# Kernel optimization log

Measured on AMD Instinct MI355X. Metric: run time of the kernel, lower is better.

## Reference

```python
import jax, jax.numpy as jnp
import numpy as np

# Dimensions matching init_kwargs
B, S, D, d_feat, O = 64, 1024, 64, 2, 10
L = S // 2  # label_site
STD = 0.01  # 'random_eye' init noise scale


def setup_inputs() -> dict:
    key = jax.random.key(0)
    k1, k2, k3, k4 = jax.random.split(key, 4)
    x = jax.random.normal(k1, (B, S, d_feat), dtype=jnp.float32)
    # InputRegion tensors, bond_str 'slri': eye over (l, r) broadcast over (s, i)
    W_left = jnp.eye(D, dtype=jnp.float32)[None, :, :, None] \
        + STD * jax.random.normal(k2, (L, D, D, d_feat), dtype=jnp.float32)
    W_right = jnp.eye(D, dtype=jnp.float32)[None, :, :, None] \
        + STD * jax.random.normal(k3, (S - L, D, D, d_feat), dtype=jnp.float32)
    # OutputSite tensor, bond_str 'olr': eye over (l, r) broadcast over o
    out_core = jnp.eye(D, dtype=jnp.float32)[None, :, :] \
        + STD * jax.random.normal(k4, (O, D, D), dtype=jnp.float32)
    return {"x": x, "W_left": W_left, "out_core": out_core, "W_right": W_right}


def reference(x, W_left, out_core, W_right):
    # x: [B, S, d]; W_left: [L, D, D, d]; out_core: [O, D, D]; W_right: [S-L, D, D, d]
    Ls = W_left.shape[0]
    Dv = W_left.shape[1]
    Bv = x.shape[0]
    # Per-site matrices (einsum 'slri,bsi->bslr'), laid out scan-major [S, B, D, D]
    mats_l = jnp.einsum('slri,bsi->sblr', W_left, x[:, :Ls])
    mats_r = jnp.einsum('slri,bsi->sblr', W_right, x[:, Ls:])
    # Open boundary edge vectors e = [1, 0, ..., 0]
    e = jnp.zeros((Dv,), dtype=x.dtype).at[0].set(1.0)
    v0 = jnp.broadcast_to(e, (Bv, Dv))
    # Left-to-right vector propagation through left chain
    def lstep(v, m):
        return jnp.einsum('bl,blr->br', v, m), None
    vL, _ = jax.lax.scan(lstep, v0, mats_l)
    # Right-to-left vector propagation through right chain
    def rstep(w, m):
        return jnp.einsum('blr,br->bl', m, w), None
    wR, _ = jax.lax.scan(rstep, v0, mats_r, reverse=True)
    # Contract through the output core: [B, O]
    return jnp.einsum('bl,olr,br->bo', vL, out_core, wR)
```

## Files before the change

### kernel.cpp

```cpp
#include <hip/hip_runtime.h>
#include <stdint.h>

#define NSITE 512
#define DD    64
#define NB    64
#define NO    10
#define NSEG  16
#define SEGLEN 32
#define SLAB_BYTES 32768
#define PACK_BYTES 16384

typedef short bf16x8 __attribute__((ext_vector_type(8)));
typedef float f32x16 __attribute__((ext_vector_type(16)));

__device__ __forceinline__ uint32_t pk2(float a, float b) {
    return __builtin_amdgcn_perm(__float_as_uint(b), __float_as_uint(a), 0x07060302);
}

__device__ __forceinline__ float2 pkmul2(float2 a, float2 b) {
    float2 r;
    asm("v_pk_mul_f32 %0, %1, %2" : "=v"(r) : "v"(a), "v"(b));
    return r;
}

__global__ __launch_bounds__(256) void pack_kernel(float* __restrict__ wl,
                                                   float* __restrict__ wr) {
    const int g = blockIdx.x;
    const int right = (g >= NSITE) ? 1 : 0;
    const int s = right ? g - NSITE : g;
    float* base = (right ? wr : wl) + (size_t)s * (SLAB_BYTES / 4);

    __shared__ float2 st[DD * 65];
    const float4* src4 = (const float4*)base;
    for (int e4 = threadIdx.x; e4 < DD * DD / 2; e4 += 256) {
        const float4 v = src4[e4];
        const int e = e4 * 2;
        float2* d = &st[(e >> 6) * 65 + (e & 63)];
        d[0] = make_float2(v.x, v.y);
        d[1] = make_float2(v.z, v.w);
    }
    __syncthreads();

    uint32_t* out = (uint32_t*)base;
    #pragma unroll
    for (int rr = 0; rr < 16; ++rr) {
        const int od = rr * 256 + threadIdx.x;
        const int chunk = od >> 8, i = chunk >> 3, sk = chunk & 7;
        const int H = (od >> 7) & 1, m5 = (od >> 2) & 31, d = od & 3;
        const int m = 32 * i + m5, k = 8 * sk + 4 * H + d;
        const float2 a = right ? st[m * 65 + k] : st[k * 65 + m];
        out[od] = pk2(a.x, a.y);
    }
}

__device__ __forceinline__ void dma16(const void* gp, void* lp) {
    __builtin_amdgcn_global_load_lds(
        (const __attribute__((address_space(1))) uint32_t*)gp,
        (__attribute__((address_space(3))) uint32_t*)lp, 16, 0, 0);
}

__global__ __launch_bounds__(256, 2) void stage1_kernel(
        const float* __restrict__ x, float* __restrict__ wl, float* __restrict__ wr) {
    const int pb   = blockIdx.x;
    const int bid  = (pb & 7) * 64 + (pb >> 3);
    const int side = bid >> 8;
    const int seg  = (bid >> 4) & 15;
    const int bq   = bid & 15;
    const int wave = threadIdx.x >> 6;
    const int lane = threadIdx.x & 63;
    const int b    = bq * 4 + wave;
    const int m5   = lane & 31;
    const int H    = lane >> 5;

    __shared__ __align__(16) char ring[4][PACK_BYTES];
    __shared__ float2 xs[4][SEGLEN];

    char* wbuf = (char*)(side ? wr : wl);

    if (lane < SEGLEN) {
        const float2* xp = ((const float2*)x) + (size_t)b * 1024 + (side ? NSITE : 0);
        const int sg = seg * SEGLEN + (side ? SEGLEN - 1 - lane : lane);
        xs[wave][lane] = xp[sg];
    }

    auto siteAddr = [&](int t) -> const char* {
        const int sg = seg * SEGLEN + (side ? SEGLEN - 1 - t : t);
        return wbuf + (size_t)sg * SLAB_BYTES;
    };

    #pragma unroll
    for (int t0 = 0; t0 < 2; ++t0) {
        const char* sb = siteAddr(t0);
        #pragma unroll
        for (int c = 0; c < 4; ++c) {
            const int ch = wave * 4 + c;
            dma16(sb + ch * 1024 + lane * 16, ring[t0] + ch * 1024);
        }
    }

    f32x16 acc[2][2];
    #pragma unroll
    for (int i = 0; i < 2; ++i)
        #pragma unroll
        for (int j = 0; j < 2; ++j)
            #pragma unroll
            for (int q = 0; q < 16; ++q) {
                const int row = (q & 3) + 8 * (q >> 2) + 4 * H;
                acc[i][j][q] = (i == j && row == m5) ? 1.f : 0.f;
            }

    f32x16 zf;
    #pragma unroll
    for (int q = 0; q < 16; ++q) zf[q] = 0.f;

    union BU { bf16x8 v; uint32_t w[4]; };

    for (int t = 0; t < SEGLEN; ++t) {
        int t2 = t + 2; if (t2 > SEGLEN - 1) t2 = SEGLEN - 1;
        {
            const char* sb = siteAddr(t2);
            char* lb = ring[(t + 2) & 3];
            #pragma unroll
            for (int c = 0; c < 4; ++c) {
                const int ch = wave * 4 + c;
                dma16(sb + ch * 1024 + lane * 16, lb + ch * 1024);
            }
        }
        asm volatile("s_waitcnt vmcnt(8)" ::: "memory");
        asm volatile("s_barrier" ::: "memory");

        const char* rb = ring[t & 3];
        const float2 xv = xs[wave][t];
        const float2 xx = make_float2(xv.x, xv.x);
        const float2 xy = make_float2(xv.y, xv.y);

        BU bfa[8][2];
        #pragma unroll
        for (int sk = 0; sk < 8; ++sk) {
            const int mi = sk >> 2, qb = 4 * (sk & 3);
            #pragma unroll
            for (int j = 0; j < 2; ++j)
                #pragma unroll
                for (int dp = 0; dp < 2; ++dp) {
                    const float2 v01 = make_float2(acc[mi][j][qb + 2 * dp],
                                                   acc[mi][j][qb + 2 * dp + 1]);
                    const float2 pa = pkmul2(xx, v01);
                    const float2 pb = pkmul2(xy, v01);
                    bfa[sk][j].w[2 * dp + 0] = pk2(pa.x, pb.x);
                    bfa[sk][j].w[2 * dp + 1] = pk2(pa.y, pb.y);
                }
        }

        __builtin_amdgcn_s_setprio(1);
        #pragma unroll
        for (int sk = 0; sk < 8; ++sk) {
            #pragma unroll
            for (int i = 0; i < 2; ++i) {
                union { bf16x8 v; uint4 u; } a;
                a.u = *(const uint4*)(rb + (i * 8 + sk) * 1024 + lane * 16);
                #pragma unroll
                for (int j = 0; j < 2; ++j)
                    acc[i][j] = __builtin_amdgcn_mfma_f32_32x32x16_bf16(
                        a.v, bfa[sk][j].v, (sk == 0) ? zf : acc[i][j], 0, 0, 0);
            }
        }
        __builtin_amdgcn_s_setprio(0);
    }

    {
        const int p = b * NSEG + seg;
        char* pdst = wbuf + (size_t)(p >> 1) * SLAB_BYTES + PACK_BYTES + (p & 1) * 8192;
        #pragma unroll
        for (int i = 0; i < 2; ++i)
            #pragma unroll
            for (int j = 0; j < 2; ++j) {
                const int c = 32 * j + m5;
                #pragma unroll
                for (int Q = 0; Q < 4; ++Q) {
                    const int r0 = 32 * i + 8 * Q + 4 * H;
                    uint2 val;
                    val.x = pk2(acc[i][j][4 * Q + 0], acc[i][j][4 * Q + 1]);
                    val.y = pk2(acc[i][j][4 * Q + 2], acc[i][j][4 * Q + 3]);
                    *(uint2*)(pdst + c * 128 + r0 * 2) = val;
                }
            }
    }
    asm volatile("s_waitcnt vmcnt(0)" ::: "memory");
}

__global__ __launch_bounds__(512) void tail_kernel(
        const float* __restrict__ wl, const float* __restrict__ wr,
        const float* __restrict__ core, float* __restrict__ out) {
    const int b    = blockIdx.x;
    const int tid  = threadIdx.x;
    const int side = tid >> 8;
    const int r    = tid & 63;
    const int cg   = (tid >> 6) & 3;
    const char* wbuf = (const char*)(side ? wr : wl);

    __shared__ float vsh[2][DD];
    __shared__ float part[2][4][DD];
    if ((tid & 255) < DD) vsh[side][r] = (r == 0) ? 1.f : 0.f;

    auto Pseg = [&](int gi) -> const uint16_t* {
        const int g = side ? (NSEG - 1 - gi) : gi;
        const int p = b * NSEG + g;
        return (const uint16_t*)(wbuf
            + (size_t)(p >> 1) * SLAB_BYTES + PACK_BYTES + (p & 1) * 8192);
    };

    float pv[16];
    {
        const uint16_t* P = Pseg(0);
        #pragma unroll
        for (int cc = 0; cc < 16; ++cc)
            pv[cc] = __uint_as_float(((uint32_t)P[(cg * 16 + cc) * 64 + r]) << 16);
    }
    __syncthreads();

    for (int gi = 0; gi < NSEG; ++gi) {
        float nv[16];
        const bool more = (gi + 1 < NSEG);
        if (more) {
            const uint16_t* Pn = Pseg(gi + 1);
            #pragma unroll
            for (int cc = 0; cc < 16; ++cc)
                nv[cc] = __uint_as_float(((uint32_t)Pn[(cg * 16 + cc) * 64 + r]) << 16);
        }
        float acc = 0.f;
        #pragma unroll
        for (int cc = 0; cc < 16; ++cc)
            acc = fmaf(vsh[side][cg * 16 + cc], pv[cc], acc);
        part[side][cg][r] = acc;
        asm volatile("s_waitcnt lgkmcnt(0)" ::: "memory");
        __builtin_amdgcn_s_barrier();
        if ((tid & 255) < DD)
            vsh[side][r] = part[side][0][r] + part[side][1][r]
                         + part[side][2][r] + part[side][3][r];
        asm volatile("s_waitcnt lgkmcnt(0)" ::: "memory");
        __builtin_amdgcn_s_barrier();
        if (more) {
            #pragma unroll
            for (int cc = 0; cc < 16; ++cc) pv[cc] = nv[cc];
        }
    }
    const int wv   = tid >> 6;
    const int lane = tid & 63;
    const float wrv = vsh[1][lane];
    for (int o = wv; o < NO; o += 8) {
        float acc = 0.f;
        #pragma unroll 8
        for (int l = 0; l < DD; ++l)
            acc += vsh[0][l] * core[(o * DD + l) * DD + lane];
        acc *= wrv;
        #pragma unroll
        for (int off = 32; off > 0; off >>= 1)
            acc += __shfl_xor(acc, off, 64);
        if (lane == 0) out[b * NO + o] = acc;
    }
}

extern "C" void kernel_launch(void* const* d_in, const int* in_sizes, int n_in,
                              void* d_out, int out_size, void* d_ws, size_t ws_size,
                              hipStream_t stream) {
    const float* x    = (const float*)d_in[0];
    float*       wl   = (float*)d_in[1];
    const float* core = (const float*)d_in[2];
    float*       wr   = (float*)d_in[3];

    pack_kernel<<<2 * NSITE, 256, 0, stream>>>(wl, wr);
    stage1_kernel<<<512, 256, 0, stream>>>(x, wl, wr);
    tail_kernel<<<NB, 512, 0, stream>>>(wl, wr, core, (float*)d_out);
}
```

Baseline: 166.6 us.

## Fuse weight packing into stage1 with per-group atomic spin barrier

Removes the separate pack kernel. Each stage1 block now transposes and packs two weight sites in place into bf16. A per-group atomic counter barrier then waits until all 16 blocks in the segment group have finished packing before stage1 streams the packed slabs. This targets a kernel launch boundary and the end-of-kernel drain. In exchange it adds a memset launch, a spin-wait that relies on all 512 blocks being co-resident, and extra LDS and register pressure at the start of stage1.

After: 254.4 us. +52.7%, slower.

```diff
diff --git a/kernel.cpp b/kernel.cpp
--- a/kernel.cpp
+++ b/kernel.cpp
@@ -23,36 +23,6 @@
     return r;
 }
 
-__global__ __launch_bounds__(256) void pack_kernel(float* __restrict__ wl,
-                                                   float* __restrict__ wr) {
-    const int g = blockIdx.x;
-    const int right = (g >= NSITE) ? 1 : 0;
-    const int s = right ? g - NSITE : g;
-    float* base = (right ? wr : wl) + (size_t)s * (SLAB_BYTES / 4);
-
-    __shared__ float2 st[DD * 65];
-    const float4* src4 = (const float4*)base;
-    for (int e4 = threadIdx.x; e4 < DD * DD / 2; e4 += 256) {
-        const float4 v = src4[e4];
-        const int e = e4 * 2;
-        float2* d = &st[(e >> 6) * 65 + (e & 63)];
-        d[0] = make_float2(v.x, v.y);
-        d[1] = make_float2(v.z, v.w);
-    }
-    __syncthreads();
-
-    uint32_t* out = (uint32_t*)base;
-    #pragma unroll
-    for (int rr = 0; rr < 16; ++rr) {
-        const int od = rr * 256 + threadIdx.x;
-        const int chunk = od >> 8, i = chunk >> 3, sk = chunk & 7;
-        const int H = (od >> 7) & 1, m5 = (od >> 2) & 31, d = od & 3;
-        const int m = 32 * i + m5, k = 8 * sk + 4 * H + d;
-        const float2 a = right ? st[m * 65 + k] : st[k * 65 + m];
-        out[od] = pk2(a.x, a.y);
-    }
-}
-
 __device__ __forceinline__ void dma16(const void* gp, void* lp) {
     __builtin_amdgcn_global_load_lds(
         (const __attribute__((address_space(1))) uint32_t*)gp,
@@ -60,7 +30,8 @@
 }
 
 __global__ __launch_bounds__(256, 2) void stage1_kernel(
-        const float* __restrict__ x, float* __restrict__ wl, float* __restrict__ wr) {
+        const float* __restrict__ x, float* __restrict__ wl, float* __restrict__ wr,
+        int* grpcnt) {
     const int pb   = blockIdx.x;
     const int bid  = (pb & 7) * 64 + (pb >> 3);
     const int side = bid >> 8;
@@ -76,6 +47,44 @@
     __shared__ float2 xs[4][SEGLEN];
 
     char* wbuf = (char*)(side ? wr : wl);
+
+    {
+        float2* st = (float2*)ring;
+        #pragma unroll
+        for (int rep = 0; rep < 2; ++rep) {
+            const int s = seg * SEGLEN + 2 * bq + rep;
+            float* base = (float*)wbuf + (size_t)s * (SLAB_BYTES / 4);
+            const float4* src4 = (const float4*)base;
+            for (int e4 = threadIdx.x; e4 < DD * DD / 2; e4 += 256) {
+                const float4 v = src4[e4];
+                const int e = e4 * 2;
+                float2* d = &st[(e >> 6) * 65 + (e & 63)];
+                d[0] = make_float2(v.x, v.y);
+                d[1] = make_float2(v.z, v.w);
+            }
+            __syncthreads();
+            uint32_t* outp = (uint32_t*)base;
+            #pragma unroll
+            for (int rr = 0; rr < 16; ++rr) {
+                const int od = rr * 256 + threadIdx.x;
+                const int chunk = od >> 8, i2 = chunk >> 3, sk = chunk & 7;
+                const int Hh = (od >> 7) & 1, mm5 = (od >> 2) & 31, dd = od & 3;
+                const int m = 32 * i2 + mm5, k = 8 * sk + 4 * Hh + dd;
+                const float2 a = side ? st[m * 65 + k] : st[k * 65 + m];
+                outp[od] = pk2(a.x, a.y);
+            }
+            __syncthreads();
+        }
+        __threadfence();
+        __syncthreads();
+        if (threadIdx.x == 0) {
+            const int g = bid >> 4;
+            atomicAdd(&grpcnt[g], 1);
+            while (atomicAdd(&grpcnt[g], 0) < 16) { }
+        }
+        __syncthreads();
+        __threadfence();
+    }
 
     if (lane < SEGLEN) {
         const float2* xp = ((const float2*)x) + (size_t)b * 1024 + (side ? NSITE : 0);
@@ -267,8 +276,9 @@
     float*       wl   = (float*)d_in[1];
     const float* core = (const float*)d_in[2];
     float*       wr   = (float*)d_in[3];
-
-    pack_kernel<<<2 * NSITE, 256, 0, stream>>>(wl, wr);
-    stage1_kernel<<<512, 256, 0, stream>>>(x, wl, wr);
+    int* grpcnt = (int*)d_ws;
+
+    hipMemsetAsync(grpcnt, 0, 32 * sizeof(int), stream);
+    stage1_kernel<<<512, 256, 0, stream>>>(x, wl, wr, grpcnt);
     tail_kernel<<<NB, 512, 0, stream>>>(wl, wr, core, (float*)d_out);
 }
```
